# Kernel optimization log

Hardware: AMD Instinct MI355X
Metric: run time of the kernel (lower is better)

Reference implementation:

```python
import jax, jax.numpy as jnp
import numpy as np

IN, OUT, S = 4096, 4096, 256
B, T = 4, 2048

# Straight-through-estimator sign quantizer (binary quant of low-rank factors).
@jax.custom_vjp
def ste_sign(x):
    return jnp.sign(x)

def _ste_fwd(x):
    return jnp.sign(x), None

def _ste_bwd(_, g):
    return (g,)

ste_sign.defvjp(_ste_fwd, _ste_bwd)


def setup_inputs() -> dict:
    key = jax.random.key(0)
    ks = jax.random.split(key, 14)
    nrm = lambda k, shp, s: jax.random.normal(k, shp, dtype=jnp.float32) * s
    uni = lambda k, shp: jax.random.uniform(k, shp, dtype=jnp.float32, minval=0.1, maxval=1.0)
    return {
        "x": nrm(ks[0], (B, T, IN), 1.0),
        "V": nrm(ks[1], (S, IN), 0.02),
        "U": nrm(ks[2], (OUT, S), 0.02),
        "v1": uni(ks[3], (1, S)),
        "v2": uni(ks[4], (1, IN)),
        "u1": uni(ks[5], (1, OUT)),
        "u2": uni(ks[6], (1, S)),
        "V_R": nrm(ks[7], (S, IN), 0.02),
        "U_R": nrm(ks[8], (OUT, S), 0.02),
        "v1_R": uni(ks[9], (1, S)),
        "v2_R": uni(ks[10], (1, IN)),
        "u1_R": uni(ks[11], (1, OUT)),
        "u2_R": uni(ks[12], (1, S)),
        "bias": nrm(ks[13], (OUT,), 0.02),
    }


def _branch(x2, V, U, v1, v2, u1, u2):
    # y = (((x * v2) @ sign(V).T) * (v1*u2)) @ sign(U).T * u1   (left-to-right, as in torch)
    Vq = ste_sign(V)          # [S, IN]
    Uq = ste_sign(U)          # [OUT, S]
    h = (x2 * v2) @ Vq.T      # [N, S]
    h = h * (v1 * u2)         # per-rank scale
    y = h @ Uq.T              # [N, OUT]
    return y * u1


def reference(x, V, U, v1, v2, u1, u2, V_R, U_R, v1_R, v2_R, u1_R, u2_R, bias):
    shp = x.shape
    x2 = x.reshape(-1, shp[-1])                                  # [N, IN]
    y = _branch(x2, V, U, v1, v2, u1, u2)
    y = y + _branch(x2, V_R, U_R, v1_R, v2_R, u1_R, u2_R)        # residual low-rank branch
    y = y + bias
    return y.reshape(shp[:-1] + (OUT,))
```

## Files before the change

### kernel.cpp

```cpp
#include <hip/hip_runtime.h>
#include <hip/hip_bf16.h>
#include <stdint.h>
#include <stddef.h>

typedef __attribute__((ext_vector_type(8))) short short8;
typedef __attribute__((ext_vector_type(4))) float floatx4;

#define AS_GLOBAL(p) (const __attribute__((address_space(1))) void*)(p)
#define AS_LDS(p)    (__attribute__((address_space(3))) void*)(p)

static constexpr int IN_DIM  = 4096;
static constexpr int OUT_DIM = 4096;
static constexpr int S_DIM   = 256;
static constexpr int S2      = 512;


__global__ void build_w1_kernel(const float* __restrict__ V, const float* __restrict__ v2,
                                const float* __restrict__ V_R, const float* __restrict__ v2_R,
                                __hip_bfloat16* __restrict__ W1) {
  const int idx4 = (blockIdx.x * 256 + threadIdx.x) * 4;
  const int i = idx4 & (IN_DIM - 1);
  const int s = idx4 >> 12;
  floatx4 w, sc;
  if (s < S_DIM) {
    w  = *(const floatx4*)(V + s * IN_DIM + i);
    sc = *(const floatx4*)(v2 + i);
  } else {
    w  = *(const floatx4*)(V_R + (s - S_DIM) * IN_DIM + i);
    sc = *(const floatx4*)(v2_R + i);
  }
  union { ushort4 v; __hip_bfloat16 h[4]; } u;
#pragma unroll
  for (int j = 0; j < 4; ++j) {
    const float sg = (w[j] > 0.f) ? 1.f : ((w[j] < 0.f) ? -1.f : 0.f);
    u.h[j] = __float2bfloat16(sg * sc[j]);
  }
  *(ushort4*)((unsigned short*)W1 + idx4) = u.v;
}

__global__ void build_w2_kernel(const float* __restrict__ U, const float* __restrict__ u1,
                                const float* __restrict__ v1, const float* __restrict__ u2,
                                const float* __restrict__ U_R, const float* __restrict__ u1_R,
                                const float* __restrict__ v1_R, const float* __restrict__ u2_R,
                                __hip_bfloat16* __restrict__ W2) {
  const int idx4 = (blockIdx.x * 256 + threadIdx.x) * 4;
  const int s = idx4 & (S2 - 1);
  const int o = idx4 >> 9;
  floatx4 w, scs;
  float sco;
  if (s < S_DIM) {
    w   = *(const floatx4*)(U + o * S_DIM + s);
    sco = u1[o];
    const floatx4 a = *(const floatx4*)(v1 + s);
    const floatx4 b = *(const floatx4*)(u2 + s);
    scs = a * b;
  } else {
    const int ss = s - S_DIM;
    w   = *(const floatx4*)(U_R + o * S_DIM + ss);
    sco = u1_R[o];
    const floatx4 a = *(const floatx4*)(v1_R + ss);
    const floatx4 b = *(const floatx4*)(u2_R + ss);
    scs = a * b;
  }
  union { ushort4 v; __hip_bfloat16 h[4]; } u;
#pragma unroll
  for (int j = 0; j < 4; ++j) {
    const float sg = (w[j] > 0.f) ? 1.f : ((w[j] < 0.f) ? -1.f : 0.f);
    u.h[j] = __float2bfloat16(sg * sco * scs[j]);
  }
  *(ushort4*)((unsigned short*)W2 + idx4) = u.v;
}

__global__ void cvt_x_kernel(const float* __restrict__ x, __hip_bfloat16* __restrict__ xb) {
  const int idx = blockIdx.x * 256 + threadIdx.x;
  const floatx4 f0 = *((const floatx4*)x + idx * 2);
  const floatx4 f1 = *((const floatx4*)x + idx * 2 + 1);
  union { short8 v; __hip_bfloat16 h[8]; } u;
  u.h[0] = __float2bfloat16(f0.x); u.h[1] = __float2bfloat16(f0.y);
  u.h[2] = __float2bfloat16(f0.z); u.h[3] = __float2bfloat16(f0.w);
  u.h[4] = __float2bfloat16(f1.x); u.h[5] = __float2bfloat16(f1.y);
  u.h[6] = __float2bfloat16(f1.z); u.h[7] = __float2bfloat16(f1.w);
  *((short8*)xb + idx) = u.v;
}

__global__ __launch_bounds__(256, 2)
void gemm1_kernel(const __hip_bfloat16* __restrict__ A,
                  const __hip_bfloat16* __restrict__ B,
                  __hip_bfloat16* __restrict__ C) {
  constexpr int K = IN_DIM;
  constexpr int N = S2;
  constexpr int BM = 128, BN = 64, BK = 64;

  __shared__ __hip_bfloat16 As[BM * BK];
  __shared__ __hip_bfloat16 Bs[BN * BK];

  const int t = threadIdx.x;
  const int wave = t >> 6;
  const int lane = t & 63;
  const int r16 = lane & 15;
  const int quad = lane >> 4;

  const int f = blockIdx.x;
  const int c = f & 7;
  const int l = f >> 3;
  const int tm0 = (c * 8 + (l >> 3)) * BM;
  const int tn0 = (l & 7) * BN;

  const int wm = (wave & 1) * 64;
  const int wn = (wave >> 1) * 32;

  floatx4 acc[4][2] = {};

  for (int k0 = 0; k0 < K; k0 += BK) {
#pragma unroll
    for (int i = 0; i < 4; ++i) {
      const int p = t + i * 256;
      const int row = p >> 3;
      const int ql = (p & 7) ^ (row & 7);
      const __hip_bfloat16* gp = A + (size_t)(tm0 + row) * K + k0 + ql * 8;
      __builtin_amdgcn_global_load_lds(AS_GLOBAL(gp), AS_LDS((char*)As + p * 16), 16, 0, 0);
    }
#pragma unroll
    for (int i = 0; i < 2; ++i) {
      const int p = t + i * 256;
      const int row = p >> 3;
      const int ql = (p & 7) ^ (row & 7);
      const __hip_bfloat16* gp = B + (size_t)(tn0 + row) * K + k0 + ql * 8;
      __builtin_amdgcn_global_load_lds(AS_GLOBAL(gp), AS_LDS((char*)Bs + p * 16), 16, 0, 0);
    }
    __syncthreads();

#pragma unroll
    for (int ks = 0; ks < 2; ++ks) {
      short8 a[4], b[2];
      const int cc = ks * 4 + quad;
#pragma unroll
      for (int i = 0; i < 4; ++i) {
        const int ar = wm + i * 16 + r16;
        a[i] = *reinterpret_cast<const short8*>((const char*)As + (ar * 8 + (cc ^ (ar & 7))) * 16);
      }
#pragma unroll
      for (int j = 0; j < 2; ++j) {
        const int br = wn + j * 16 + r16;
        b[j] = *reinterpret_cast<const short8*>((const char*)Bs + (br * 8 + (cc ^ (br & 7))) * 16);
      }
#pragma unroll
      for (int i = 0; i < 4; ++i)
#pragma unroll
        for (int j = 0; j < 2; ++j)
          acc[i][j] = __builtin_amdgcn_mfma_f32_16x16x32_bf16(a[i], b[j], acc[i][j], 0, 0, 0);
    }
    __syncthreads();
  }

#pragma unroll
  for (int i = 0; i < 4; ++i)
#pragma unroll
    for (int j = 0; j < 2; ++j)
#pragma unroll
      for (int r = 0; r < 4; ++r) {
        const int row = tm0 + wm + i * 16 + quad * 4 + r;
        const int col = tn0 + wn + j * 16 + r16;
        C[(size_t)row * N + col] = __float2bfloat16(acc[i][j][r]);
      }
}

__global__ __launch_bounds__(256, 2)
void gemm2_kernel(const __hip_bfloat16* __restrict__ A,
                  const __hip_bfloat16* __restrict__ B,
                  const float* __restrict__ bias,
                  float* __restrict__ C) {
  constexpr int K = S2;
  constexpr int N = OUT_DIM;
  constexpr int BM = 128, BN = 128, BK = 64;

  __shared__ __hip_bfloat16 As[BM * BK];
  __shared__ __hip_bfloat16 Bs[BN * BK];

  const int t = threadIdx.x;
  const int wave = t >> 6;
  const int lane = t & 63;
  const int r16 = lane & 15;
  const int quad = lane >> 4;

  const int f = blockIdx.x;
  const int c = f & 7;
  const int l = f >> 3;
  const int tm0 = (c * 8 + (l >> 5)) * BM;
  const int tn0 = (l & 31) * BN;

  const int wm = (wave & 1) * 64;
  const int wn = (wave >> 1) * 64;

  floatx4 acc[4][4] = {};

  for (int k0 = 0; k0 < K; k0 += BK) {
#pragma unroll
    for (int i = 0; i < 4; ++i) {
      const int p = t + i * 256;
      const int row = p >> 3;
      const int ql = (p & 7) ^ (row & 7);
      const __hip_bfloat16* gp = A + (size_t)(tm0 + row) * K + k0 + ql * 8;
      __builtin_amdgcn_global_load_lds(AS_GLOBAL(gp), AS_LDS((char*)As + p * 16), 16, 0, 0);
    }
#pragma unroll
    for (int i = 0; i < 4; ++i) {
      const int p = t + i * 256;
      const int row = p >> 3;
      const int ql = (p & 7) ^ (row & 7);
      const __hip_bfloat16* gp = B + (size_t)(tn0 + row) * K + k0 + ql * 8;
      __builtin_amdgcn_global_load_lds(AS_GLOBAL(gp), AS_LDS((char*)Bs + p * 16), 16, 0, 0);
    }
    __syncthreads();

#pragma unroll
    for (int ks = 0; ks < 2; ++ks) {
      short8 a[4], b[4];
      const int cc = ks * 4 + quad;
#pragma unroll
      for (int i = 0; i < 4; ++i) {
        const int ar = wm + i * 16 + r16;
        a[i] = *reinterpret_cast<const short8*>((const char*)As + (ar * 8 + (cc ^ (ar & 7))) * 16);
      }
#pragma unroll
      for (int j = 0; j < 4; ++j) {
        const int br = wn + j * 16 + r16;
        b[j] = *reinterpret_cast<const short8*>((const char*)Bs + (br * 8 + (cc ^ (br & 7))) * 16);
      }
#pragma unroll
      for (int i = 0; i < 4; ++i)
#pragma unroll
        for (int j = 0; j < 4; ++j)
          acc[i][j] = __builtin_amdgcn_mfma_f32_16x16x32_bf16(a[i], b[j], acc[i][j], 0, 0, 0);
    }
    __syncthreads();
  }

  float bi[4];
#pragma unroll
  for (int j = 0; j < 4; ++j) bi[j] = bias[tn0 + wn + j * 16 + r16];

#pragma unroll
  for (int i = 0; i < 4; ++i)
#pragma unroll
    for (int j = 0; j < 4; ++j)
#pragma unroll
      for (int r = 0; r < 4; ++r) {
        const int row = tm0 + wm + i * 16 + quad * 4 + r;
        const int col = tn0 + wn + j * 16 + r16;
        C[(size_t)row * N + col] = acc[i][j][r] + bi[j];
      }
}

extern "C" void kernel_launch(void* const* d_in, const int* in_sizes, int n_in,
                              void* d_out, int out_size, void* d_ws, size_t ws_size,
                              hipStream_t stream) {
  const float* x    = (const float*)d_in[0];
  const float* V    = (const float*)d_in[1];
  const float* U    = (const float*)d_in[2];
  const float* v1   = (const float*)d_in[3];
  const float* v2   = (const float*)d_in[4];
  const float* u1   = (const float*)d_in[5];
  const float* u2   = (const float*)d_in[6];
  const float* V_R  = (const float*)d_in[7];
  const float* U_R  = (const float*)d_in[8];
  const float* v1_R = (const float*)d_in[9];
  const float* v2_R = (const float*)d_in[10];
  const float* u1_R = (const float*)d_in[11];
  const float* u2_R = (const float*)d_in[12];
  const float* bias = (const float*)d_in[13];
  float* out = (float*)d_out;

  const int M = in_sizes[0] / IN_DIM;

  char* ws = (char*)d_ws;
  __hip_bfloat16* W1 = (__hip_bfloat16*)ws;
  __hip_bfloat16* W2 = (__hip_bfloat16*)(ws + (size_t)4 * 1024 * 1024);
  __hip_bfloat16* H  = (__hip_bfloat16*)(ws + (size_t)8 * 1024 * 1024);
  __hip_bfloat16* Xb = (__hip_bfloat16*)(ws + (size_t)16 * 1024 * 1024);

  build_w1_kernel<<<(S2 * IN_DIM) / 1024, 256, 0, stream>>>(V, v2, V_R, v2_R, W1);
  build_w2_kernel<<<(OUT_DIM * S2) / 1024, 256, 0, stream>>>(U, u1, v1, u2, U_R, u1_R, v1_R, u2_R, W2);
  cvt_x_kernel<<<(M * IN_DIM) / (8 * 256), 256, 0, stream>>>(x, Xb);

  gemm1_kernel<<<(M / 128) * (S2 / 64), 256, 0, stream>>>(Xb, W1, H);

  gemm2_kernel<<<(M / 128) * (OUT_DIM / 128), 256, 0, stream>>>(H, W2, bias, out);
}
```

Before: 351.1 us.

## Double-buffer gemm1 LDS tiles and merge prep kernels into one launch

Merges the three preprocessing kernels (W1 build, W2 build, x conversion) into a single launch that branches on block index, saving two kernel launches. In gemm1 the LDS tiles are now double-buffered, so the next K-tile is issued with global_load_lds while the current one feeds the MFMAs, keeping one barrier per iteration. gemm2 launch bounds go from 2 to 3 blocks per SM, which may limit registers. The double-buffered LDS doubles shared memory use in gemm1, and no wait separates the async prefetch from the reads of the other buffer, so correctness relies on the trailing barrier ordering the loads.

```diff
diff --git a/kernel.cpp b/kernel.cpp
--- a/kernel.cpp
+++ b/kernel.cpp
@@ -14,73 +14,74 @@
 static constexpr int S_DIM   = 256;
 static constexpr int S2      = 512;
 
-
-__global__ void build_w1_kernel(const float* __restrict__ V, const float* __restrict__ v2,
-                                const float* __restrict__ V_R, const float* __restrict__ v2_R,
-                                __hip_bfloat16* __restrict__ W1) {
-  const int idx4 = (blockIdx.x * 256 + threadIdx.x) * 4;
-  const int i = idx4 & (IN_DIM - 1);
-  const int s = idx4 >> 12;
-  floatx4 w, sc;
-  if (s < S_DIM) {
-    w  = *(const floatx4*)(V + s * IN_DIM + i);
-    sc = *(const floatx4*)(v2 + i);
+__global__ void prep_kernel(const float* __restrict__ V, const float* __restrict__ v2,
+                            const float* __restrict__ V_R, const float* __restrict__ v2_R,
+                            const float* __restrict__ U, const float* __restrict__ u1,
+                            const float* __restrict__ v1, const float* __restrict__ u2,
+                            const float* __restrict__ U_R, const float* __restrict__ u1_R,
+                            const float* __restrict__ v1_R, const float* __restrict__ u2_R,
+                            const float* __restrict__ x,
+                            __hip_bfloat16* __restrict__ W1,
+                            __hip_bfloat16* __restrict__ W2,
+                            __hip_bfloat16* __restrict__ Xb) {
+  const int bid = blockIdx.x;
+  if (bid < 2048) {
+    const int idx4 = (bid * 256 + threadIdx.x) * 4;
+    const int i = idx4 & (IN_DIM - 1);
+    const int s = idx4 >> 12;
+    floatx4 w, sc;
+    if (s < S_DIM) {
+      w  = *(const floatx4*)(V + s * IN_DIM + i);
+      sc = *(const floatx4*)(v2 + i);
+    } else {
+      w  = *(const floatx4*)(V_R + (s - S_DIM) * IN_DIM + i);
+      sc = *(const floatx4*)(v2_R + i);
+    }
+    union { ushort4 v; __hip_bfloat16 h[4]; } u;
+#pragma unroll
+    for (int j = 0; j < 4; ++j) {
+      const float sg = (w[j] > 0.f) ? 1.f : ((w[j] < 0.f) ? -1.f : 0.f);
+      u.h[j] = __float2bfloat16(sg * sc[j]);
+    }
+    *(ushort4*)((unsigned short*)W1 + idx4) = u.v;
+  } else if (bid < 4096) {
+    const int idx4 = ((bid - 2048) * 256 + threadIdx.x) * 4;
+    const int s = idx4 & (S2 - 1);
+    const int o = idx4 >> 9;
+    floatx4 w, scs;
+    float sco;
+    if (s < S_DIM) {
+      w   = *(const floatx4*)(U + o * S_DIM + s);
+      sco = u1[o];
+      const floatx4 a = *(const floatx4*)(v1 + s);
+      const floatx4 b = *(const floatx4*)(u2 + s);
+      scs = a * b;
+    } else {
+      const int ss = s - S_DIM;
+      w   = *(const floatx4*)(U_R + o * S_DIM + ss);
+      sco = u1_R[o];
+      const floatx4 a = *(const floatx4*)(v1_R + ss);
+      const floatx4 b = *(const floatx4*)(u2_R + ss);
+      scs = a * b;
+    }
+    union { ushort4 v; __hip_bfloat16 h[4]; } u;
+#pragma unroll
+    for (int j = 0; j < 4; ++j) {
+      const float sg = (w[j] > 0.f) ? 1.f : ((w[j] < 0.f) ? -1.f : 0.f);
+      u.h[j] = __float2bfloat16(sg * sco * scs[j]);
+    }
+    *(ushort4*)((unsigned short*)W2 + idx4) = u.v;
   } else {
-    w  = *(const floatx4*)(V_R + (s - S_DIM) * IN_DIM + i);
-    sc = *(const floatx4*)(v2_R + i);
+    const int idx = (bid - 4096) * 256 + threadIdx.x;
+    const floatx4 f0 = *((const floatx4*)x + idx * 2);
+    const floatx4 f1 = *((const floatx4*)x + idx * 2 + 1);
+    union { short8 v; __hip_bfloat16 h[8]; } u;
+    u.h[0] = __float2bfloat16(f0.x); u.h[1] = __float2bfloat16(f0.y);
+    u.h[2] = __float2bfloat16(f0.z); u.h[3] = __float2bfloat16(f0.w);
+    u.h[4] = __float2bfloat16(f1.x); u.h[5] = __float2bfloat16(f1.y);
+    u.h[6] = __float2bfloat16(f1.z); u.h[7] = __float2bfloat16(f1.w);
+    *((short8*)Xb + idx) = u.v;
   }
-  union { ushort4 v; __hip_bfloat16 h[4]; } u;
-#pragma unroll
-  for (int j = 0; j < 4; ++j) {
-    const float sg = (w[j] > 0.f) ? 1.f : ((w[j] < 0.f) ? -1.f : 0.f);
-    u.h[j] = __float2bfloat16(sg * sc[j]);
-  }
-  *(ushort4*)((unsigned short*)W1 + idx4) = u.v;
-}
-
-__global__ void build_w2_kernel(const float* __restrict__ U, const float* __restrict__ u1,
-                                const float* __restrict__ v1, const float* __restrict__ u2,
-                                const float* __restrict__ U_R, const float* __restrict__ u1_R,
-                                const float* __restrict__ v1_R, const float* __restrict__ u2_R,
-                                __hip_bfloat16* __restrict__ W2) {
-  const int idx4 = (blockIdx.x * 256 + threadIdx.x) * 4;
-  const int s = idx4 & (S2 - 1);
-  const int o = idx4 >> 9;
-  floatx4 w, scs;
-  float sco;
-  if (s < S_DIM) {
-    w   = *(const floatx4*)(U + o * S_DIM + s);
-    sco = u1[o];
-    const floatx4 a = *(const floatx4*)(v1 + s);
-    const floatx4 b = *(const floatx4*)(u2 + s);
-    scs = a * b;
-  } else {
-    const int ss = s - S_DIM;
-    w   = *(const floatx4*)(U_R + o * S_DIM + ss);
-    sco = u1_R[o];
-    const floatx4 a = *(const floatx4*)(v1_R + ss);
-    const floatx4 b = *(const floatx4*)(u2_R + ss);
-    scs = a * b;
-  }
-  union { ushort4 v; __hip_bfloat16 h[4]; } u;
-#pragma unroll
-  for (int j = 0; j < 4; ++j) {
-    const float sg = (w[j] > 0.f) ? 1.f : ((w[j] < 0.f) ? -1.f : 0.f);
-    u.h[j] = __float2bfloat16(sg * sco * scs[j]);
-  }
-  *(ushort4*)((unsigned short*)W2 + idx4) = u.v;
-}
-
-__global__ void cvt_x_kernel(const float* __restrict__ x, __hip_bfloat16* __restrict__ xb) {
-  const int idx = blockIdx.x * 256 + threadIdx.x;
-  const floatx4 f0 = *((const floatx4*)x + idx * 2);
-  const floatx4 f1 = *((const floatx4*)x + idx * 2 + 1);
-  union { short8 v; __hip_bfloat16 h[8]; } u;
-  u.h[0] = __float2bfloat16(f0.x); u.h[1] = __float2bfloat16(f0.y);
-  u.h[2] = __float2bfloat16(f0.z); u.h[3] = __float2bfloat16(f0.w);
-  u.h[4] = __float2bfloat16(f1.x); u.h[5] = __float2bfloat16(f1.y);
-  u.h[6] = __float2bfloat16(f1.z); u.h[7] = __float2bfloat16(f1.w);
-  *((short8*)xb + idx) = u.v;
 }
 
 __global__ __launch_bounds__(256, 2)
@@ -91,8 +92,8 @@
   constexpr int N = S2;
   constexpr int BM = 128, BN = 64, BK = 64;
 
-  __shared__ __hip_bfloat16 As[BM * BK];
-  __shared__ __hip_bfloat16 Bs[BN * BK];
+  __shared__ __hip_bfloat16 As[2][BM * BK];
+  __shared__ __hip_bfloat16 Bs[2][BN * BK];
 
   const int t = threadIdx.x;
   const int wave = t >> 6;
@@ -111,14 +112,18 @@
 
   floatx4 acc[4][2] = {};
 
-  for (int k0 = 0; k0 < K; k0 += BK) {
+  const int pa_row = t >> 3;
+  const int pa_ql0 = (t & 7);
+  const int pb_row = t >> 3;
+
+  auto stage = [&](int buf, int k0) {
 #pragma unroll
     for (int i = 0; i < 4; ++i) {
       const int p = t + i * 256;
       const int row = p >> 3;
       const int ql = (p & 7) ^ (row & 7);
       const __hip_bfloat16* gp = A + (size_t)(tm0 + row) * K + k0 + ql * 8;
-      __builtin_amdgcn_global_load_lds(AS_GLOBAL(gp), AS_LDS((char*)As + p * 16), 16, 0, 0);
+      __builtin_amdgcn_global_load_lds(AS_GLOBAL(gp), AS_LDS((char*)&As[buf][0] + p * 16), 16, 0, 0);
     }
 #pragma unroll
     for (int i = 0; i < 2; ++i) {
@@ -126,10 +131,19 @@
       const int row = p >> 3;
       const int ql = (p & 7) ^ (row & 7);
       const __hip_bfloat16* gp = B + (size_t)(tn0 + row) * K + k0 + ql * 8;
-      __builtin_amdgcn_global_load_lds(AS_GLOBAL(gp), AS_LDS((char*)Bs + p * 16), 16, 0, 0);
-    }
-    __syncthreads();
-
+      __builtin_amdgcn_global_load_lds(AS_GLOBAL(gp), AS_LDS((char*)&Bs[buf][0] + p * 16), 16, 0, 0);
+    }
+  };
+
+  stage(0, 0);
+  __syncthreads();
+
+  int buf = 0;
+  for (int k0 = 0; k0 < K; k0 += BK) {
+    if (k0 + BK < K) stage(buf ^ 1, k0 + BK);
+
+    const char* as = (const char*)&As[buf][0];
+    const char* bs = (const char*)&Bs[buf][0];
 #pragma unroll
     for (int ks = 0; ks < 2; ++ks) {
       short8 a[4], b[2];
@@ -137,12 +151,12 @@
 #pragma unroll
       for (int i = 0; i < 4; ++i) {
         const int ar = wm + i * 16 + r16;
-        a[i] = *reinterpret_cast<const short8*>((const char*)As + (ar * 8 + (cc ^ (ar & 7))) * 16);
+        a[i] = *reinterpret_cast<const short8*>(as + (ar * 8 + (cc ^ (ar & 7))) * 16);
       }
 #pragma unroll
       for (int j = 0; j < 2; ++j) {
         const int br = wn + j * 16 + r16;
-        b[j] = *reinterpret_cast<const short8*>((const char*)Bs + (br * 8 + (cc ^ (br & 7))) * 16);
+        b[j] = *reinterpret_cast<const short8*>(bs + (br * 8 + (cc ^ (br & 7))) * 16);
       }
 #pragma unroll
       for (int i = 0; i < 4; ++i)
@@ -151,6 +165,7 @@
           acc[i][j] = __builtin_amdgcn_mfma_f32_16x16x32_bf16(a[i], b[j], acc[i][j], 0, 0, 0);
     }
     __syncthreads();
+    buf ^= 1;
   }
 
 #pragma unroll
@@ -165,7 +180,7 @@
       }
 }
 
-__global__ __launch_bounds__(256, 2)
+__global__ __launch_bounds__(256, 3)
 void gemm2_kernel(const __hip_bfloat16* __restrict__ A,
                   const __hip_bfloat16* __restrict__ B,
                   const float* __restrict__ bias,
@@ -279,9 +294,9 @@
   __hip_bfloat16* H  = (__hip_bfloat16*)(ws + (size_t)8 * 1024 * 1024);
   __hip_bfloat16* Xb = (__hip_bfloat16*)(ws + (size_t)16 * 1024 * 1024);
 
-  build_w1_kernel<<<(S2 * IN_DIM) / 1024, 256, 0, stream>>>(V, v2, V_R, v2_R, W1);
-  build_w2_kernel<<<(OUT_DIM * S2) / 1024, 256, 0, stream>>>(U, u1, v1, u2, U_R, u1_R, v1_R, u2_R, W2);
-  cvt_x_kernel<<<(M * IN_DIM) / (8 * 256), 256, 0, stream>>>(x, Xb);
+  const int cvt_blocks = (M * IN_DIM) / (8 * 256);
+  prep_kernel<<<4096 + cvt_blocks, 256, 0, stream>>>(
+      V, v2, V_R, v2_R, U, u1, v1, u2, U_R, u1_R, v1_R, u2_R, x, W1, W2, Xb);
 
   gemm1_kernel<<<(M / 128) * (S2 / 64), 256, 0, stream>>>(Xb, W1, H);
 
```

Result: no change. 345.4 us (-1.6%).
